# Performance work log

Hardware: AMD Instinct MI355X
Metric: run time of the kernel (lower is better)

The kernel has to match this reference:

```python
import jax, jax.numpy as jnp
import numpy as np

B, S, D_IN, D_OUT, HID, E, SHARE, TOPK = 4, 2048, 1024, 1024, 2048, 8, 1, 2


def setup_inputs() -> dict:
    key = jax.random.key(0)
    ks = jax.random.split(key, 12)
    s_in = 1.0 / np.sqrt(D_IN)
    s_hid = 1.0 / np.sqrt(HID)
    return {
        "x": jax.random.normal(ks[0], (B, S, D_IN), jnp.float32),
        "gate_w": jax.random.normal(ks[1], (D_IN, E), jnp.float32) * s_in,
        "gate_b": jnp.zeros((E,), jnp.float32),
        "ew1": jax.random.normal(ks[2], (E, D_IN, HID), jnp.float32) * s_in,
        "eb1": jnp.zeros((E, HID), jnp.float32),
        "ew2": jax.random.normal(ks[3], (E, HID, D_OUT), jnp.float32) * s_hid,
        "eb2": jnp.zeros((E, D_OUT), jnp.float32),
        "sw1": jax.random.normal(ks[4], (SHARE, D_IN, HID), jnp.float32) * s_in,
        "sb1": jnp.zeros((SHARE, HID), jnp.float32),
        "sw2": jax.random.normal(ks[5], (SHARE, HID, D_OUT), jnp.float32) * s_hid,
        "sb2": jnp.zeros((SHARE, D_OUT), jnp.float32),
        "top_k": TOPK,
    }


def reference(x, gate_w, gate_b, ew1, eb1, ew2, eb2, sw1, sb1, sw2, sb2, top_k):
    Bx, Sx, Din = x.shape
    flat_x = x.reshape(-1, Din)                      # [T, D]
    T = flat_x.shape[0]
    Ex = gate_w.shape[1]

    # gate + softmax + top-k, renormalize top-k weights
    logits = flat_x @ gate_w + gate_b                # [T, E]
    expert_weights = jax.nn.softmax(logits, axis=-1)
    topv, topi = jax.lax.top_k(expert_weights, top_k)
    topv = topv / jnp.sum(topv, axis=-1, keepdims=True)

    # per-token combine weights scattered into [T, E] (zero for unselected)
    combine = jnp.zeros((T, Ex), flat_x.dtype)
    combine = combine.at[jnp.arange(T)[:, None], topi].add(topv)

    # expert MLPs (BasicExpert: Linear -> ReLU -> Linear), batched over experts
    h = jax.nn.relu(jnp.einsum("td,edh->teh", flat_x, ew1) + eb1)   # [T, E, H]
    eo = jnp.einsum("teh,eho->teo", h, ew2) + eb2                    # [T, E, O]
    moe_out = jnp.einsum("teo,te->to", eo, combine)                  # [T, O]
    final = moe_out.reshape(Bx, Sx, -1)

    # shared experts added densely to every token
    for k in range(sw1.shape[0]):
        sh = jax.nn.relu(jnp.einsum("bsd,dh->bsh", x, sw1[k]) + sb1[k])
        final = final + jnp.einsum("bsh,ho->bso", sh, sw2[k]) + sb2[k]

    return final, expert_weights
```

## Files before the change

### kernel.cpp

```cpp
#include <hip/hip_runtime.h>
#include <hip/hip_bf16.h>
#include <stdint.h>

#define T_TOK 8192
#define DIN   1024
#define DOUT  1024
#define HID   2048
#define NEXP  8
#define MAXN  8192

typedef __attribute__((ext_vector_type(8))) short short8;
typedef __attribute__((ext_vector_type(4))) float floatx4;

__device__ __forceinline__ ushort f2bf(float f) {
    uint32_t u = __float_as_uint(f);
    uint32_t r = (u + 0x7fffu + ((u >> 16) & 1u)) >> 16;
    return (ushort)r;
}

__device__ __forceinline__ void load_lds_16(const ushort* g, ushort* l) {
    __builtin_amdgcn_global_load_lds(
        (const __attribute__((address_space(1))) void*)g,
        (__attribute__((address_space(3))) void*)l, 16, 0, 0);
}

__global__ void convert_x_kernel(const float* __restrict__ in, ushort* __restrict__ out, int n4) {
    int i = blockIdx.x * blockDim.x + threadIdx.x;
    if (i >= n4) return;
    float4 v = ((const float4*)in)[i];
    ushort4 o;
    o.x = f2bf(v.x); o.y = f2bf(v.y); o.z = f2bf(v.z); o.w = f2bf(v.w);
    ((ushort4*)out)[i] = o;
}

__global__ void transpose_bf16_kernel(const float* __restrict__ in, ushort* __restrict__ out,
                                      int R, int C) {
    __shared__ float tile[64][65];
    size_t base = (size_t)blockIdx.z * R * C;
    in  += base;
    out += base;
    int r0 = blockIdx.y * 64, c0 = blockIdx.x * 64;
    int t  = threadIdx.x;
    int rr = t >> 4;
    int cc = (t & 15) * 4;
    for (int p = 0; p < 4; p++) {
        int row = rr + p * 16;
        float4 v = *(const float4*)(in + (size_t)(r0 + row) * C + c0 + cc);
        tile[row][cc + 0] = v.x; tile[row][cc + 1] = v.y;
        tile[row][cc + 2] = v.z; tile[row][cc + 3] = v.w;
    }
    __syncthreads();
    for (int p = 0; p < 4; p++) {
        int orow = rr + p * 16;
        ushort4 o;
        o.x = f2bf(tile[cc + 0][orow]);
        o.y = f2bf(tile[cc + 1][orow]);
        o.z = f2bf(tile[cc + 2][orow]);
        o.w = f2bf(tile[cc + 3][orow]);
        *(ushort4*)(out + (size_t)(c0 + orow) * R + r0 + cc) = o;
    }
}

__global__ void gate_compute_kernel(const float* __restrict__ x, const float* __restrict__ gw,
                                    const float* __restrict__ gb, float* __restrict__ ew_out,
                                    int* __restrict__ te1, int* __restrict__ te2,
                                    float* __restrict__ tw1, float* __restrict__ tw2) {
    int gid  = blockIdx.x * blockDim.x + threadIdx.x;
    int t    = gid >> 6;
    int lane = threadIdx.x & 63;
    if (t >= T_TOK) return;
    float acc[8];
    #pragma unroll
    for (int e = 0; e < 8; e++) acc[e] = 0.f;
    const float* xrow = x + (size_t)t * DIN;
    #pragma unroll
    for (int i = 0; i < 16; i++) {
        int d = lane + i * 64;
        float xv = xrow[d];
        const float4* wr = (const float4*)(gw + (size_t)d * 8);
        float4 w0 = wr[0], w1 = wr[1];
        acc[0] += xv * w0.x; acc[1] += xv * w0.y; acc[2] += xv * w0.z; acc[3] += xv * w0.w;
        acc[4] += xv * w1.x; acc[5] += xv * w1.y; acc[6] += xv * w1.z; acc[7] += xv * w1.w;
    }
    #pragma unroll
    for (int e = 0; e < 8; e++)
        #pragma unroll
        for (int off = 32; off; off >>= 1) acc[e] += __shfl_xor(acc[e], off);
    if (lane == 0) {
        float l[8], mx = -1e30f;
        #pragma unroll
        for (int e = 0; e < 8; e++) { l[e] = acc[e] + gb[e]; mx = fmaxf(mx, l[e]); }
        float s = 0.f;
        #pragma unroll
        for (int e = 0; e < 8; e++) { l[e] = expf(l[e] - mx); s += l[e]; }
        float inv = 1.f / s;
        #pragma unroll
        for (int e = 0; e < 8; e++) { l[e] *= inv; ew_out[(size_t)t * 8 + e] = l[e]; }
        int i1 = 0;
        #pragma unroll
        for (int e = 1; e < 8; e++) if (l[e] > l[i1]) i1 = e;
        int i2 = (i1 == 0) ? 1 : 0;
        #pragma unroll
        for (int e = 0; e < 8; e++) if (e != i1 && l[e] > l[i2]) i2 = e;
        float s2 = l[i1] + l[i2];
        te1[t] = i1; tw1[t] = l[i1] / s2;
        te2[t] = i2; tw2[t] = l[i2] / s2;
    }
}

__global__ void build_lists_kernel(const int* __restrict__ te1, const int* __restrict__ te2,
                                   const float* __restrict__ tw1, const float* __restrict__ tw2,
                                   int* __restrict__ counts, int* __restrict__ etok,
                                   float* __restrict__ ew) {
    __shared__ int lcnt[NEXP];
    __shared__ int gbase[NEXP];
    int tid = threadIdx.x;
    int t = blockIdx.x * 256 + tid;
    if (tid < NEXP) lcnt[tid] = 0;
    __syncthreads();
    int e1 = te1[t], e2 = te2[t];
    float w1 = tw1[t], w2 = tw2[t];
    int r1 = atomicAdd(&lcnt[e1], 1);
    int r2 = atomicAdd(&lcnt[e2], 1);
    __syncthreads();
    if (tid < NEXP) gbase[tid] = atomicAdd(&counts[tid], lcnt[tid]);
    __syncthreads();
    int s1 = gbase[e1] + r1;
    etok[e1 * MAXN + s1] = t;
    ew  [e1 * MAXN + s1] = w1;
    int s2 = gbase[e2] + r2;
    etok[e2 * MAXN + s2] = t;
    ew  [e2 * MAXN + s2] = w2;
}

__global__ void prefix_kernel(const int* __restrict__ counts, int* __restrict__ offsets) {
    if (threadIdx.x == 0 && blockIdx.x == 0) {
        int o = 0;
        for (int e = 0; e < NEXP; e++) { offsets[e] = o; o += counts[e]; }
    }
}

template <int LAYER>
__global__ __launch_bounds__(256)
void gemm_kernel(const ushort* __restrict__ A, const ushort* __restrict__ BtE,
                 const ushort* __restrict__ BtS,
                 const float* __restrict__ biasE, const float* __restrict__ biasS,
                 ushort* __restrict__ Hout, float* __restrict__ Out,
                 const int* __restrict__ counts, const int* __restrict__ offsets,
                 const int* __restrict__ etok, const float* __restrict__ eww) {
    constexpr int K    = (LAYER == 1) ? DIN : HID;
    constexpr int N    = (LAYER == 1) ? HID : DOUT;
    constexpr int NB_N = N / 128;
    constexpr int RB   = NEXP * (MAXN / 128) * NB_N;

    const int bid = (int)blockIdx.x;
    const bool routed = bid < RB;
    int e = 0, m0, n0, cnt, rowbase = 0;
    const ushort* Bt;
    const float* bcol;
    if (routed) {
        e = bid & 7;
        int r = bid >> 3;
        m0 = (r / NB_N) * 128;
        n0 = (r % NB_N) * 128;
        cnt = counts[e];
        if (m0 >= cnt) return;
        rowbase = offsets[e];
        Bt = BtE + (size_t)e * N * K;
        bcol = biasE + (size_t)e * N;
    } else {
        int r = bid - RB;
        m0 = (r / NB_N) * 128;
        n0 = (r % NB_N) * 128;
        cnt = T_TOK;
        Bt = BtS;
        bcol = biasS;
    }

    __shared__ ushort As[8192];
    __shared__ ushort Bs[8192];
    __shared__ int    rowA[128];

    const int tid = threadIdx.x;
    if (tid < 128) {
        int g = m0 + tid;
        int row;
        if constexpr (LAYER == 1) {
            row = routed ? ((g < cnt) ? etok[e * MAXN + g] : 0) : g;
        } else {
            row = routed ? (rowbase + ((g < cnt) ? g : 0)) : (T_TOK * 2 + g);
        }
        rowA[tid] = row;
    }
    __syncthreads();

    const int wave = tid >> 6, lane = tid & 63;
    const int lm = lane & 15, lq = lane >> 4;

    const ushort* gA[4];
    const ushort* gB[4];
    ushort* dA[4];
    ushort* dB[4];
    #pragma unroll
    for (int i = 0; i < 4; i++) {
        int b = wave * 4 + i;
        int rblk = b >> 1, kkb = b & 1;
        int r = rblk * 16 + lm;
        gA[i] = A + (size_t)rowA[r] * K + kkb * 32 + lq * 8;
        gB[i] = Bt + (size_t)(n0 + r) * K + kkb * 32 + lq * 8;
        dA[i] = &As[b * 512];
        dB[i] = &Bs[b * 512];
    }

    floatx4 acc[4][4];
    #pragma unroll
    for (int i = 0; i < 4; i++)
        #pragma unroll
        for (int j = 0; j < 4; j++) acc[i][j] = (floatx4){0.f, 0.f, 0.f, 0.f};

    for (int k0 = 0; k0 < K; k0 += 64) {
        #pragma unroll
        for (int i = 0; i < 4; i++) {
            load_lds_16(gA[i] + k0, dA[i]);
            load_lds_16(gB[i] + k0, dB[i]);
        }
        __syncthreads();
        #pragma unroll
        for (int kkb = 0; kkb < 2; kkb++) {
            short8 afr[4], bfr[4];
            #pragma unroll
            for (int mt = 0; mt < 4; mt++)
                afr[mt] = *(const short8*)&As[(((wave >> 1) * 4 + mt) * 2 + kkb) * 512 + lane * 8];
            #pragma unroll
            for (int nt = 0; nt < 4; nt++)
                bfr[nt] = *(const short8*)&Bs[(((wave & 1) * 4 + nt) * 2 + kkb) * 512 + lane * 8];
            #pragma unroll
            for (int mt = 0; mt < 4; mt++)
                #pragma unroll
                for (int nt = 0; nt < 4; nt++)
                    acc[mt][nt] = __builtin_amdgcn_mfma_f32_16x16x32_bf16(
                        afr[mt], bfr[nt], acc[mt][nt], 0, 0, 0);
        }
        __syncthreads();
    }

    const int wm = (wave >> 1) * 64, wn = (wave & 1) * 64;
    #pragma unroll
    for (int mt = 0; mt < 4; mt++) {
        int rl_base = wm + mt * 16 + lq * 4;
        #pragma unroll
        for (int nt = 0; nt < 4; nt++) {
            int col = n0 + wn + nt * 16 + lm;
            float bv = bcol[col];
            #pragma unroll
            for (int r = 0; r < 4; r++) {
                int rl = rl_base + r;
                int g  = m0 + rl;
                float v = acc[mt][nt][r];
                if constexpr (LAYER == 1) {
                    if (!routed || g < cnt) {
                        v = fmaxf(v + bv, 0.f);
                        int orow = routed ? (rowbase + g) : (T_TOK * 2 + g);
                        Hout[(size_t)orow * HID + col] = f2bf(v);
                    }
                } else {
                    if (routed) {
                        if (g < cnt) {
                            int   tok = etok[e * MAXN + g];
                            float w   = eww[e * MAXN + g];
                            atomicAdd(&Out[(size_t)tok * DOUT + col], (v + bv) * w);
                        }
                    } else {
                        atomicAdd(&Out[(size_t)g * DOUT + col], v + bv);
                    }
                }
            }
        }
    }
}

extern "C" void kernel_launch(void* const* d_in, const int* in_sizes, int n_in,
                              void* d_out, int out_size, void* d_ws, size_t ws_size,
                              hipStream_t stream) {
    const float* x   = (const float*)d_in[0];
    const float* gw  = (const float*)d_in[1];
    const float* gb  = (const float*)d_in[2];
    const float* ew1 = (const float*)d_in[3];
    const float* eb1 = (const float*)d_in[4];
    const float* ew2 = (const float*)d_in[5];
    const float* eb2 = (const float*)d_in[6];
    const float* sw1 = (const float*)d_in[7];
    const float* sb1 = (const float*)d_in[8];
    const float* sw2 = (const float*)d_in[9];
    const float* sb2 = (const float*)d_in[10];

    float* out_final = (float*)d_out;
    float* out_ew    = out_final + (size_t)T_TOK * DOUT;

    char* ws = (char*)d_ws;
    size_t off = 0;
    auto alloc = [&](size_t bytes) -> void* {
        void* p = ws + off;
        off += (bytes + 255) & ~(size_t)255;
        return p;
    };
    ushort* x_bf    = (ushort*)alloc((size_t)T_TOK * DIN * 2);
    ushort* ew1t    = (ushort*)alloc((size_t)NEXP * HID * DIN * 2);
    ushort* ew2t    = (ushort*)alloc((size_t)NEXP * DOUT * HID * 2);
    ushort* sw1t    = (ushort*)alloc((size_t)HID * DIN * 2);
    ushort* sw2t    = (ushort*)alloc((size_t)DOUT * HID * 2);
    ushort* h_all   = (ushort*)alloc((size_t)T_TOK * 3 * HID * 2);
    int*    counts  = (int*)alloc(NEXP * 4);
    int*    offsets = (int*)alloc(NEXP * 4);
    int*    etok    = (int*)alloc((size_t)NEXP * MAXN * 4);
    float*  eww     = (float*)alloc((size_t)NEXP * MAXN * 4);
    int*    te1     = (int*)alloc((size_t)T_TOK * 4);
    int*    te2     = (int*)alloc((size_t)T_TOK * 4);
    float*  tw1     = (float*)alloc((size_t)T_TOK * 4);
    float*  tw2     = (float*)alloc((size_t)T_TOK * 4);

    hipMemsetAsync(d_out, 0, (size_t)T_TOK * DOUT * 4, stream);
    hipMemsetAsync(counts, 0, NEXP * 4, stream);

    convert_x_kernel<<<(T_TOK * DIN / 4) / 256, 256, 0, stream>>>(x, x_bf, T_TOK * DIN / 4);
    transpose_bf16_kernel<<<dim3(HID / 64, DIN / 64, NEXP), 256, 0, stream>>>(ew1, ew1t, DIN, HID);
    transpose_bf16_kernel<<<dim3(DOUT / 64, HID / 64, NEXP), 256, 0, stream>>>(ew2, ew2t, HID, DOUT);
    transpose_bf16_kernel<<<dim3(HID / 64, DIN / 64, 1), 256, 0, stream>>>(sw1, sw1t, DIN, HID);
    transpose_bf16_kernel<<<dim3(DOUT / 64, HID / 64, 1), 256, 0, stream>>>(sw2, sw2t, HID, DOUT);

    gate_compute_kernel<<<T_TOK / 4, 256, 0, stream>>>(x, gw, gb, out_ew, te1, te2, tw1, tw2);
    build_lists_kernel<<<T_TOK / 256, 256, 0, stream>>>(te1, te2, tw1, tw2, counts, etok, eww);
    prefix_kernel<<<1, 64, 0, stream>>>(counts, offsets);

    gemm_kernel<1><<<NEXP * 64 * 16 + 64 * 16, 256, 0, stream>>>(
        x_bf, ew1t, sw1t, eb1, sb1, h_all, nullptr, counts, offsets, etok, eww);
    gemm_kernel<2><<<NEXP * 64 * 8 + 64 * 8, 256, 0, stream>>>(
        h_all, ew2t, sw2t, eb2, sb2, nullptr, out_final, counts, offsets, etok, eww);
}
```

Before: 851.8 us.

## Compact GEMM work list and load MFMA fragments directly from global with register double-buffering

The prefix kernel now builds a compact list of (expert, m-tile) work items, so the GEMM grid no longer launches thousands of blocks that exit at once. The GEMM drops the LDS staging through global_load_lds and barriers. Each wave loads its MFMA operand fragments straight from global memory into registers, double-buffered across k-steps. Launch bounds now request 2 blocks per SM. The cost is that there is no LDS sharing, so each fragment is fetched redundantly by the two waves that use it, which raises global/L2 traffic and register pressure.

```diff
diff --git a/kernel.cpp b/kernel.cpp
--- a/kernel.cpp
+++ b/kernel.cpp
@@ -8,6 +8,7 @@
 #define HID   2048
 #define NEXP  8
 #define MAXN  8192
+#define MAXWORK 200
 
 typedef __attribute__((ext_vector_type(8))) short short8;
 typedef __attribute__((ext_vector_type(4))) float floatx4;
@@ -16,12 +17,6 @@
     uint32_t u = __float_as_uint(f);
     uint32_t r = (u + 0x7fffu + ((u >> 16) & 1u)) >> 16;
     return (ushort)r;
-}
-
-__device__ __forceinline__ void load_lds_16(const ushort* g, ushort* l) {
-    __builtin_amdgcn_global_load_lds(
-        (const __attribute__((address_space(1))) void*)g,
-        (__attribute__((address_space(3))) void*)l, 16, 0, 0);
 }
 
 __global__ void convert_x_kernel(const float* __restrict__ in, ushort* __restrict__ out, int n4) {
@@ -133,84 +128,64 @@
     ew  [e2 * MAXN + s2] = w2;
 }
 
-__global__ void prefix_kernel(const int* __restrict__ counts, int* __restrict__ offsets) {
+__global__ void prefix_kernel(const int* __restrict__ counts, int* __restrict__ offsets,
+                              int* __restrict__ work, int* __restrict__ nwork) {
     if (threadIdx.x == 0 && blockIdx.x == 0) {
         int o = 0;
         for (int e = 0; e < NEXP; e++) { offsets[e] = o; o += counts[e]; }
+        int nw = 0;
+        for (int s = 0; s < MAXN / 128; s++)
+            for (int e = 0; e < NEXP; e++)
+                if (s * 128 < counts[e]) work[nw++] = (e << 16) | s;
+        for (int s = 0; s < T_TOK / 128; s++) work[nw++] = (8 << 16) | s;
+        nwork[0] = nw;
     }
 }
 
 template <int LAYER>
-__global__ __launch_bounds__(256)
+__global__ __launch_bounds__(256, 2)
 void gemm_kernel(const ushort* __restrict__ A, const ushort* __restrict__ BtE,
                  const ushort* __restrict__ BtS,
                  const float* __restrict__ biasE, const float* __restrict__ biasS,
                  ushort* __restrict__ Hout, float* __restrict__ Out,
                  const int* __restrict__ counts, const int* __restrict__ offsets,
-                 const int* __restrict__ etok, const float* __restrict__ eww) {
+                 const int* __restrict__ etok, const float* __restrict__ eww,
+                 const int* __restrict__ work, const int* __restrict__ nwork) {
     constexpr int K    = (LAYER == 1) ? DIN : HID;
     constexpr int N    = (LAYER == 1) ? HID : DOUT;
     constexpr int NB_N = N / 128;
-    constexpr int RB   = NEXP * (MAXN / 128) * NB_N;
-
-    const int bid = (int)blockIdx.x;
-    const bool routed = bid < RB;
-    int e = 0, m0, n0, cnt, rowbase = 0;
-    const ushort* Bt;
-    const float* bcol;
-    if (routed) {
-        e = bid & 7;
-        int r = bid >> 3;
-        m0 = (r / NB_N) * 128;
-        n0 = (r % NB_N) * 128;
-        cnt = counts[e];
-        if (m0 >= cnt) return;
-        rowbase = offsets[e];
-        Bt = BtE + (size_t)e * N * K;
-        bcol = biasE + (size_t)e * N;
-    } else {
-        int r = bid - RB;
-        m0 = (r / NB_N) * 128;
-        n0 = (r % NB_N) * 128;
-        cnt = T_TOK;
-        Bt = BtS;
-        bcol = biasS;
-    }
-
-    __shared__ ushort As[8192];
-    __shared__ ushort Bs[8192];
-    __shared__ int    rowA[128];
-
-    const int tid = threadIdx.x;
-    if (tid < 128) {
-        int g = m0 + tid;
+
+    const int idx  = (int)blockIdx.x;
+    const int item = idx / NB_N;
+    if (item >= nwork[0]) return;
+    const int n0 = (idx % NB_N) * 128;
+    const int w  = work[item];
+    const int e  = w >> 16;
+    const int m0 = (w & 0xffff) * 128;
+    const bool routed = (e < 8);
+    const int cnt     = routed ? counts[e] : T_TOK;
+    const int rowbase = routed ? offsets[e] : 0;
+    const ushort* Bt  = routed ? BtE + (size_t)e * N * K : BtS;
+    const float* bcol = routed ? biasE + (size_t)e * N : biasS;
+
+    const int tid = threadIdx.x, wave = tid >> 6, lane = tid & 63;
+    const int lm = lane & 15, lq = lane >> 4;
+    const int wm = (wave >> 1) * 64, wn = (wave & 1) * 64;
+
+    const ushort* pA[4];
+    const ushort* pB[4];
+    #pragma unroll
+    for (int mt = 0; mt < 4; mt++) {
+        int g  = m0 + wm + mt * 16 + lm;
+        int gc = (g < cnt) ? g : cnt - 1;
         int row;
-        if constexpr (LAYER == 1) {
-            row = routed ? ((g < cnt) ? etok[e * MAXN + g] : 0) : g;
-        } else {
-            row = routed ? (rowbase + ((g < cnt) ? g : 0)) : (T_TOK * 2 + g);
-        }
-        rowA[tid] = row;
-    }
-    __syncthreads();
-
-    const int wave = tid >> 6, lane = tid & 63;
-    const int lm = lane & 15, lq = lane >> 4;
-
-    const ushort* gA[4];
-    const ushort* gB[4];
-    ushort* dA[4];
-    ushort* dB[4];
-    #pragma unroll
-    for (int i = 0; i < 4; i++) {
-        int b = wave * 4 + i;
-        int rblk = b >> 1, kkb = b & 1;
-        int r = rblk * 16 + lm;
-        gA[i] = A + (size_t)rowA[r] * K + kkb * 32 + lq * 8;
-        gB[i] = Bt + (size_t)(n0 + r) * K + kkb * 32 + lq * 8;
-        dA[i] = &As[b * 512];
-        dB[i] = &Bs[b * 512];
-    }
+        if constexpr (LAYER == 1) row = routed ? etok[e * MAXN + gc] : g;
+        else                      row = routed ? (rowbase + gc) : (T_TOK * 2 + g);
+        pA[mt] = A + (size_t)row * K + lq * 8;
+    }
+    #pragma unroll
+    for (int nt = 0; nt < 4; nt++)
+        pB[nt] = Bt + (size_t)(n0 + wn + nt * 16 + lm) * K + lq * 8;
 
     floatx4 acc[4][4];
     #pragma unroll
@@ -218,33 +193,34 @@
         #pragma unroll
         for (int j = 0; j < 4; j++) acc[i][j] = (floatx4){0.f, 0.f, 0.f, 0.f};
 
-    for (int k0 = 0; k0 < K; k0 += 64) {
-        #pragma unroll
-        for (int i = 0; i < 4; i++) {
-            load_lds_16(gA[i] + k0, dA[i]);
-            load_lds_16(gB[i] + k0, dB[i]);
-        }
-        __syncthreads();
-        #pragma unroll
-        for (int kkb = 0; kkb < 2; kkb++) {
-            short8 afr[4], bfr[4];
-            #pragma unroll
-            for (int mt = 0; mt < 4; mt++)
-                afr[mt] = *(const short8*)&As[(((wave >> 1) * 4 + mt) * 2 + kkb) * 512 + lane * 8];
-            #pragma unroll
-            for (int nt = 0; nt < 4; nt++)
-                bfr[nt] = *(const short8*)&Bs[(((wave & 1) * 4 + nt) * 2 + kkb) * 512 + lane * 8];
-            #pragma unroll
-            for (int mt = 0; mt < 4; mt++)
-                #pragma unroll
-                for (int nt = 0; nt < 4; nt++)
-                    acc[mt][nt] = __builtin_amdgcn_mfma_f32_16x16x32_bf16(
-                        afr[mt], bfr[nt], acc[mt][nt], 0, 0, 0);
-        }
-        __syncthreads();
-    }
-
-    const int wm = (wave >> 1) * 64, wn = (wave & 1) * 64;
+    short8 fA0[4], fB0[4], fA1[4], fB1[4];
+    short8 gA0[4], gB0[4], gA1[4], gB1[4];
+
+    #define LD(Aar, Bar, k)  {                                              \
+        _Pragma("unroll")                                                   \
+        for (int i = 0; i < 4; i++) {                                       \
+            Aar[i] = *(const short8*)(pA[i] + (k));                         \
+            Bar[i] = *(const short8*)(pB[i] + (k));                         \
+        } }
+    #define MM(Aar, Bar)  {                                                 \
+        _Pragma("unroll")                                                   \
+        for (int mt = 0; mt < 4; mt++)                                      \
+            _Pragma("unroll")                                               \
+            for (int nt = 0; nt < 4; nt++)                                  \
+                acc[mt][nt] = __builtin_amdgcn_mfma_f32_16x16x32_bf16(      \
+                    Aar[mt], Bar[nt], acc[mt][nt], 0, 0, 0); }
+
+    LD(fA0, fB0, 0); LD(fA1, fB1, 32);
+    for (int k0 = 0; k0 < K; k0 += 128) {
+        LD(gA0, gB0, k0 + 64); LD(gA1, gB1, k0 + 96);
+        MM(fA0, fB0); MM(fA1, fB1);
+        int kn = (k0 + 128 < K) ? k0 + 128 : 0;
+        LD(fA0, fB0, kn); LD(fA1, fB1, kn + 32);
+        MM(gA0, gB0); MM(gA1, gB1);
+    }
+    #undef LD
+    #undef MM
+
     #pragma unroll
     for (int mt = 0; mt < 4; mt++) {
         int rl_base = wm + mt * 16 + lq * 4;
@@ -267,8 +243,8 @@
                     if (routed) {
                         if (g < cnt) {
                             int   tok = etok[e * MAXN + g];
-                            float w   = eww[e * MAXN + g];
-                            atomicAdd(&Out[(size_t)tok * DOUT + col], (v + bv) * w);
+                            float ww  = eww[e * MAXN + g];
+                            atomicAdd(&Out[(size_t)tok * DOUT + col], (v + bv) * ww);
                         }
                     } else {
                         atomicAdd(&Out[(size_t)g * DOUT + col], v + bv);
@@ -318,6 +294,8 @@
     int*    te2     = (int*)alloc((size_t)T_TOK * 4);
     float*  tw1     = (float*)alloc((size_t)T_TOK * 4);
     float*  tw2     = (float*)alloc((size_t)T_TOK * 4);
+    int*    work    = (int*)alloc(MAXWORK * 4);
+    int*    nwork   = (int*)alloc(4);
 
     hipMemsetAsync(d_out, 0, (size_t)T_TOK * DOUT * 4, stream);
     hipMemsetAsync(counts, 0, NEXP * 4, stream);
@@ -330,10 +308,10 @@
 
     gate_compute_kernel<<<T_TOK / 4, 256, 0, stream>>>(x, gw, gb, out_ew, te1, te2, tw1, tw2);
     build_lists_kernel<<<T_TOK / 256, 256, 0, stream>>>(te1, te2, tw1, tw2, counts, etok, eww);
-    prefix_kernel<<<1, 64, 0, stream>>>(counts, offsets);
-
-    gemm_kernel<1><<<NEXP * 64 * 16 + 64 * 16, 256, 0, stream>>>(
-        x_bf, ew1t, sw1t, eb1, sb1, h_all, nullptr, counts, offsets, etok, eww);
-    gemm_kernel<2><<<NEXP * 64 * 8 + 64 * 8, 256, 0, stream>>>(
-        h_all, ew2t, sw2t, eb2, sb2, nullptr, out_final, counts, offsets, etok, eww);
-}
+    prefix_kernel<<<1, 64, 0, stream>>>(counts, offsets, work, nwork);
+
+    gemm_kernel<1><<<MAXWORK * (HID / 128), 256, 0, stream>>>(
+        x_bf, ew1t, sw1t, eb1, sb1, h_all, nullptr, counts, offsets, etok, eww, work, nwork);
+    gemm_kernel<2><<<MAXWORK * (DOUT / 128), 256, 0, stream>>>(
+        h_all, ew2t, sw2t, eb2, sb2, nullptr, out_final, counts, offsets, etok, eww, work, nwork);
+}
```

Result: slower. 1.125 ms (+32.0%).
